# Kernel optimization log

Hardware: AMD Instinct MI355X
Metric: run time of the kernel (lower is better)

The kernel has to match this reference:

```python
import jax, jax.numpy as jnp
import numpy as np

N_NODES = 8192
N_EDGES = 262144
IN_DIM = 128
HID = 128
FLAT = N_NODES * HID  # 1048576


def gcn_conv(x, edge_index, W, b):
    """PyG-style GCNConv: add self-loops, symmetric deg^{-1/2} normalization,
    out[col] += norm * (x @ W)[row], plus bias."""
    N = x.shape[0]
    loop = jnp.arange(N)
    row = jnp.concatenate([edge_index[0], loop])  # source nodes
    col = jnp.concatenate([edge_index[1], loop])  # target nodes
    deg = jax.ops.segment_sum(jnp.ones_like(col, dtype=x.dtype), col, num_segments=N)
    dinv = jax.lax.rsqrt(jnp.maximum(deg, 1.0))  # deg >= 1 thanks to self-loops
    norm = dinv[row] * dinv[col]  # [E+N]
    h = x @ W  # [N, out]
    msg = h[row] * norm[:, None]  # gather
    out = jax.ops.segment_sum(msg, col, num_segments=N)  # scatter-add
    return out + b


def setup_inputs() -> dict:
    key = jax.random.key(0)
    ks = jax.random.split(key, 12)
    def lin(k, fan_in, shape):
        bound = 1.0 / np.sqrt(fan_in)
        return jax.random.uniform(k, shape, jnp.float32, -bound, bound)
    return {
        "x": jax.random.normal(ks[0], (N_NODES, IN_DIM), jnp.float32),
        "edge_index": jax.random.randint(ks[1], (2, N_EDGES), 0, N_NODES, jnp.int64 if jax.config.jax_enable_x64 else jnp.int32),
        "W1": lin(ks[2], IN_DIM, (IN_DIM, HID)),
        "b1": lin(ks[3], IN_DIM, (HID,)),
        "W2": lin(ks[4], HID, (HID, HID)),
        "b2": lin(ks[5], HID, (HID,)),
        "fc1_w": lin(ks[6], FLAT, (FLAT, HID)),
        "fc1_b": lin(ks[7], FLAT, (HID,)),
        "fc2_w": lin(ks[8], HID, (HID, HID)),
        "fc2_b": lin(ks[9], HID, (HID,)),
        "fc3_w": lin(ks[10], HID, (HID, 1)),
        "fc3_b": lin(ks[11], HID, (1,)),
    }


def reference(x, edge_index, W1, b1, W2, b2, fc1_w, fc1_b, fc2_w, fc2_b, fc3_w, fc3_b):
    e = jax.nn.relu(gcn_conv(x, edge_index, W1, b1))
    e = gcn_conv(e, edge_index, W2, b2)
    flat = e.reshape(-1)  # [N_NODES*HID]
    h = jax.nn.relu(flat @ fc1_w + fc1_b)
    h = jax.nn.relu(h @ fc2_w + fc2_b)
    q = h @ fc3_w + fc3_b  # [1]
    return q
```

## Files before the change

kernel.cpp:

```cpp
#include <hip/hip_runtime.h>

#define N_NODES 8192
#define N_EDGES 262144
#define DIM 128

__global__ void k_deg(const int* __restrict__ col, int* __restrict__ deg) {
    int e = blockIdx.x * blockDim.x + threadIdx.x;
    if (e < N_EDGES) atomicAdd(&deg[col[e]], 1);
}

__global__ __launch_bounds__(1024) void k_scan(const int* __restrict__ deg,
                                               int* __restrict__ rowptr,
                                               float* __restrict__ dinv) {
    __shared__ int part[1024];
    int t = threadIdx.x;
    int base = t * 8;
    int v[8];
    int s = 0;
    #pragma unroll
    for (int i = 0; i < 8; ++i) {
        int d = deg[base + i];
        dinv[base + i] = rsqrtf((float)d + 1.0f);
        v[i] = s; s += d;
    }
    part[t] = s;
    __syncthreads();
    for (int off = 1; off < 1024; off <<= 1) {
        int x = (t >= off) ? part[t - off] : 0;
        __syncthreads();
        part[t] += x;
        __syncthreads();
    }
    int basesum = (t == 0) ? 0 : part[t - 1];
    #pragma unroll
    for (int i = 0; i < 8; ++i) rowptr[base + i] = basesum + v[i];
    if (t == 1023) rowptr[8192] = part[1023];
}

__global__ void k_fill(const int* __restrict__ rows, const int* __restrict__ cols,
                       const int* __restrict__ rowptr, int* __restrict__ cnt,
                       int* __restrict__ srcs) {
    int e = blockIdx.x * blockDim.x + threadIdx.x;
    if (e < N_EDGES) {
        int c = cols[e];
        int p = atomicAdd(&cnt[c], 1);
        srcs[rowptr[c] + p] = rows[e];
    }
}

__global__ __launch_bounds__(256) void k_gemm(const float* __restrict__ x,
                                              const float* __restrict__ W,
                                              const float* __restrict__ dinv,
                                              float* __restrict__ out) {
    __shared__ float4 Wl[128 * 32];
    int t = threadIdx.x;
    const float4* W4 = (const float4*)W;
    for (int i = t; i < 128 * 32; i += 256) Wl[i] = W4[i];
    __syncthreads();

    int q  = t & 31;
    int rg = t >> 5;
    int row0 = blockIdx.x * 32;
    for (int p = 0; p < 4; ++p) {
        int row = row0 + p * 8 + rg;
        const float4* xr = (const float4*)(x + (size_t)row * DIM);
        float4 acc = {0.f, 0.f, 0.f, 0.f};
        #pragma unroll
        for (int k4 = 0; k4 < 32; ++k4) {
            float4 xv = xr[k4];
            float4 w0 = Wl[(k4 * 4 + 0) * 32 + q];
            float4 w1 = Wl[(k4 * 4 + 1) * 32 + q];
            float4 w2 = Wl[(k4 * 4 + 2) * 32 + q];
            float4 w3 = Wl[(k4 * 4 + 3) * 32 + q];
            acc.x += xv.x * w0.x + xv.y * w1.x + xv.z * w2.x + xv.w * w3.x;
            acc.y += xv.x * w0.y + xv.y * w1.y + xv.z * w2.y + xv.w * w3.y;
            acc.z += xv.x * w0.z + xv.y * w1.z + xv.z * w2.z + xv.w * w3.z;
            acc.w += xv.x * w0.w + xv.y * w1.w + xv.z * w2.w + xv.w * w3.w;
        }
        float s = dinv[row];
        acc.x *= s; acc.y *= s; acc.z *= s; acc.w *= s;
        ((float4*)(out + (size_t)row * DIM))[q] = acc;
    }
}

__global__ __launch_bounds__(256) void k_gather(const float* __restrict__ h,
                                                const int* __restrict__ srcs,
                                                const int* __restrict__ rowptr,
                                                const float* __restrict__ dinv,
                                                const float* __restrict__ b,
                                                float* __restrict__ out) {
    int t = threadIdx.x;
    int lane = t & 63;
    int node = blockIdx.x * 4 + (t >> 6);
    const float2* H = (const float2*)h;
    int beg = rowptr[node];
    int end = rowptr[node + 1];
    float2 acc = H[(size_t)node * 64 + lane];
    int j = beg;
    for (; j + 3 < end; j += 4) {
        int r0 = srcs[j], r1 = srcs[j + 1], r2 = srcs[j + 2], r3 = srcs[j + 3];
        float2 v0 = H[(size_t)r0 * 64 + lane];
        float2 v1 = H[(size_t)r1 * 64 + lane];
        float2 v2 = H[(size_t)r2 * 64 + lane];
        float2 v3 = H[(size_t)r3 * 64 + lane];
        acc.x += (v0.x + v1.x) + (v2.x + v3.x);
        acc.y += (v0.y + v1.y) + (v2.y + v3.y);
    }
    for (; j < end; ++j) {
        int r = srcs[j];
        float2 v = H[(size_t)r * 64 + lane];
        acc.x += v.x; acc.y += v.y;
    }
    float s = dinv[node];
    float2 bv = ((const float2*)b)[lane];
    float2 o;
    o.x = fmaxf(s * acc.x + bv.x, 0.f);
    o.y = fmaxf(s * acc.y + bv.y, 0.f);
    ((float2*)(out + (size_t)node * DIM))[lane] = o;
}

__global__ __launch_bounds__(256) void k_gfc(const float* __restrict__ h,
                                             const int* __restrict__ srcs,
                                             const int* __restrict__ rowptr,
                                             const float* __restrict__ dinv,
                                             const float* __restrict__ b,
                                             const float* __restrict__ w,
                                             float* __restrict__ facc) {
    __shared__ float oL[4][128];
    __shared__ float4 red4[4][32];
    int t = threadIdx.x;
    int lane = t & 63;
    int wid = t >> 6;
    int node = blockIdx.x * 4 + wid;
    const float2* H = (const float2*)h;
    int beg = rowptr[node];
    int end = rowptr[node + 1];
    float2 acc = H[(size_t)node * 64 + lane];
    int j = beg;
    for (; j + 3 < end; j += 4) {
        int r0 = srcs[j], r1 = srcs[j + 1], r2 = srcs[j + 2], r3 = srcs[j + 3];
        float2 v0 = H[(size_t)r0 * 64 + lane];
        float2 v1 = H[(size_t)r1 * 64 + lane];
        float2 v2 = H[(size_t)r2 * 64 + lane];
        float2 v3 = H[(size_t)r3 * 64 + lane];
        acc.x += (v0.x + v1.x) + (v2.x + v3.x);
        acc.y += (v0.y + v1.y) + (v2.y + v3.y);
    }
    for (; j < end; ++j) {
        int r = srcs[j];
        float2 v = H[(size_t)r * 64 + lane];
        acc.x += v.x; acc.y += v.y;
    }
    float s = dinv[node];
    float2 bv = ((const float2*)b)[lane];
    float2 o = { s * acc.x + bv.x, s * acc.y + bv.y };
    ((float2*)oL[wid])[lane] = o;
    __syncthreads();

    int q  = lane & 31;
    int kh = lane >> 5;
    size_t rowbase = (size_t)node * 128;
    float4 a4 = {0.f, 0.f, 0.f, 0.f};
    #pragma unroll 8
    for (int k2 = 0; k2 < 64; ++k2) {
        int k = k2 * 2 + kh;
        float ok = oL[wid][k];
        float4 wr = ((const float4*)(w + (rowbase + k) * 128))[q];
        a4.x += ok * wr.x;
        a4.y += ok * wr.y;
        a4.z += ok * wr.z;
        a4.w += ok * wr.w;
    }
    a4.x += __shfl_xor(a4.x, 32);
    a4.y += __shfl_xor(a4.y, 32);
    a4.z += __shfl_xor(a4.z, 32);
    a4.w += __shfl_xor(a4.w, 32);
    if (lane < 32) red4[wid][q] = a4;
    __syncthreads();
    if (t < 128) {
        const float* rf = (const float*)red4;
        float val = (rf[t] + rf[128 + t]) + (rf[256 + t] + rf[384 + t]);
        atomicAdd(&facc[t], val);
    }
}

__global__ __launch_bounds__(128) void k_tail(const float* __restrict__ facc,
                                              const float* __restrict__ fc1_b,
                                              const float* __restrict__ fc2_w,
                                              const float* __restrict__ fc2_b,
                                              const float* __restrict__ fc3_w,
                                              const float* __restrict__ fc3_b,
                                              float* __restrict__ out) {
    __shared__ float h1[128], red[128];
    int j = threadIdx.x;
    h1[j] = fmaxf(facc[j] + fc1_b[j], 0.f);
    __syncthreads();
    float a = 0.f;
    #pragma unroll 8
    for (int k = 0; k < 128; ++k) a += h1[k] * fc2_w[k * 128 + j];
    float h2 = fmaxf(a + fc2_b[j], 0.f);
    red[j] = h2 * fc3_w[j];
    __syncthreads();
    if (j == 0) {
        float s = 0.f;
        for (int k = 0; k < 128; ++k) s += red[k];
        out[0] = s + fc3_b[0];
    }
}

extern "C" void kernel_launch(void* const* d_in, const int* in_sizes, int n_in,
                              void* d_out, int out_size, void* d_ws, size_t ws_size,
                              hipStream_t stream) {
    const float* x     = (const float*)d_in[0];
    const int*   ei    = (const int*)d_in[1];
    const float* W1    = (const float*)d_in[2];
    const float* b1    = (const float*)d_in[3];
    const float* W2    = (const float*)d_in[4];
    const float* b2    = (const float*)d_in[5];
    const float* fc1_w = (const float*)d_in[6];
    const float* fc1_b = (const float*)d_in[7];
    const float* fc2_w = (const float*)d_in[8];
    const float* fc2_b = (const float*)d_in[9];
    const float* fc3_w = (const float*)d_in[10];
    const float* fc3_b = (const float*)d_in[11];
    const int* rows = ei;
    const int* cols = ei + N_EDGES;

    float* buf0   = (float*)d_ws;
    float* buf1   = buf0 + (size_t)N_NODES * DIM;
    int*   degi   = (int*)(buf1 + (size_t)N_NODES * DIM);
    int*   cnt    = degi + N_NODES;
    float* facc   = (float*)(cnt + N_NODES);
    float* dinv   = facc + DIM;
    int*   rowptr = (int*)(dinv + N_NODES);
    int*   srcs   = rowptr + N_NODES + 8;
    float* out    = (float*)d_out;

    hipMemsetAsync(degi, 0, (2 * N_NODES) * sizeof(int) + DIM * sizeof(float), stream);

    k_deg<<<N_EDGES / 256, 256, 0, stream>>>(cols, degi);
    k_scan<<<1, 1024, 0, stream>>>(degi, rowptr, dinv);
    k_fill<<<N_EDGES / 256, 256, 0, stream>>>(rows, cols, rowptr, cnt, srcs);

    k_gemm<<<N_NODES / 32, 256, 0, stream>>>(x, W1, dinv, buf0);
    k_gather<<<N_NODES / 4, 256, 0, stream>>>(buf0, srcs, rowptr, dinv, b1, buf1);

    k_gemm<<<N_NODES / 32, 256, 0, stream>>>(buf1, W2, dinv, buf0);
    k_gfc<<<N_NODES / 4, 256, 0, stream>>>(buf0, srcs, rowptr, dinv, b2, fc1_w, facc);

    k_tail<<<1, 128, 0, stream>>>(facc, fc1_b, fc2_w, fc2_b, fc3_w, fc3_b, out);
}
```

Baseline: 870.2 us.

## Replicate fc1 accumulators, stream weights nontemporally, vectorize gather, and use wave-level scan

Atomic adds from all 2048 blocks into one 128-float accumulator are spread over 64 replicas, which the tail kernel sums, to reduce atomic contention. The 512MB fc1 weight stream is read with nontemporal loads so it does not pollute the caches. The neighbor gather is factored into a helper that aligns the start, loads indices as int4 and keeps two accumulators. The single-block scan now uses wave shuffles in place of a shared-memory Hillis-Steele loop. Risks are extra memset and tail work, and different float summation order.

Result: faster. 838.9 us, median of 2 (-3.6%).

```diff
diff --git a/kernel.cpp b/kernel.cpp
--- a/kernel.cpp
+++ b/kernel.cpp
@@ -3,6 +3,9 @@
 #define N_NODES 8192
 #define N_EDGES 262144
 #define DIM 128
+#define NREP 64
+
+typedef float fv4 __attribute__((ext_vector_type(4)));
 
 __global__ void k_deg(const int* __restrict__ col, int* __restrict__ deg) {
     int e = blockIdx.x * blockDim.x + threadIdx.x;
@@ -12,7 +15,8 @@
 __global__ __launch_bounds__(1024) void k_scan(const int* __restrict__ deg,
                                                int* __restrict__ rowptr,
                                                float* __restrict__ dinv) {
-    __shared__ int part[1024];
+    __shared__ int wsum[16];
+    __shared__ int wpre[16];
     int t = threadIdx.x;
     int base = t * 8;
     int v[8];
@@ -23,18 +27,25 @@
         dinv[base + i] = rsqrtf((float)d + 1.0f);
         v[i] = s; s += d;
     }
-    part[t] = s;
-    __syncthreads();
-    for (int off = 1; off < 1024; off <<= 1) {
-        int x = (t >= off) ? part[t - off] : 0;
-        __syncthreads();
-        part[t] += x;
-        __syncthreads();
-    }
-    int basesum = (t == 0) ? 0 : part[t - 1];
-    #pragma unroll
-    for (int i = 0; i < 8; ++i) rowptr[base + i] = basesum + v[i];
-    if (t == 1023) rowptr[8192] = part[1023];
+    int lane = t & 63, wv = t >> 6;
+    int incl = s;
+    #pragma unroll
+    for (int off = 1; off < 64; off <<= 1) {
+        int n = __shfl_up(incl, off);
+        if (lane >= off) incl += n;
+    }
+    if (lane == 63) wsum[wv] = incl;
+    __syncthreads();
+    if (t == 0) {
+        int a = 0;
+        #pragma unroll
+        for (int i = 0; i < 16; ++i) { wpre[i] = a; a += wsum[i]; }
+        rowptr[8192] = a;
+    }
+    __syncthreads();
+    int ebase = wpre[wv] + incl - s;
+    #pragma unroll
+    for (int i = 0; i < 8; ++i) rowptr[base + i] = ebase + v[i];
 }
 
 __global__ void k_fill(const int* __restrict__ rows, const int* __restrict__ cols,
@@ -83,6 +94,35 @@
     }
 }
 
+__device__ __forceinline__ float2 gather_row(const float2* __restrict__ H,
+                                             const int* __restrict__ srcs,
+                                             int beg, int end, int node, int lane) {
+    float2 a0 = H[(size_t)node * 64 + lane];
+    float2 a1 = {0.f, 0.f};
+    int j = beg;
+    int npre = (4 - (beg & 3)) & 3;
+    if (npre > end - beg) npre = end - beg;
+    for (int p = 0; p < npre; ++p, ++j) {
+        float2 v = H[(size_t)srcs[j] * 64 + lane];
+        a0.x += v.x; a0.y += v.y;
+    }
+    for (; j + 3 < end; j += 4) {
+        int4 s4 = *reinterpret_cast<const int4*>(srcs + j);
+        float2 v0 = H[(size_t)s4.x * 64 + lane];
+        float2 v1 = H[(size_t)s4.y * 64 + lane];
+        float2 v2 = H[(size_t)s4.z * 64 + lane];
+        float2 v3 = H[(size_t)s4.w * 64 + lane];
+        a0.x += v0.x + v2.x; a0.y += v0.y + v2.y;
+        a1.x += v1.x + v3.x; a1.y += v1.y + v3.y;
+    }
+    for (; j < end; ++j) {
+        float2 v = H[(size_t)srcs[j] * 64 + lane];
+        a1.x += v.x; a1.y += v.y;
+    }
+    a0.x += a1.x; a0.y += a1.y;
+    return a0;
+}
+
 __global__ __launch_bounds__(256) void k_gather(const float* __restrict__ h,
                                                 const int* __restrict__ srcs,
                                                 const int* __restrict__ rowptr,
@@ -92,25 +132,7 @@
     int t = threadIdx.x;
     int lane = t & 63;
     int node = blockIdx.x * 4 + (t >> 6);
-    const float2* H = (const float2*)h;
-    int beg = rowptr[node];
-    int end = rowptr[node + 1];
-    float2 acc = H[(size_t)node * 64 + lane];
-    int j = beg;
-    for (; j + 3 < end; j += 4) {
-        int r0 = srcs[j], r1 = srcs[j + 1], r2 = srcs[j + 2], r3 = srcs[j + 3];
-        float2 v0 = H[(size_t)r0 * 64 + lane];
-        float2 v1 = H[(size_t)r1 * 64 + lane];
-        float2 v2 = H[(size_t)r2 * 64 + lane];
-        float2 v3 = H[(size_t)r3 * 64 + lane];
-        acc.x += (v0.x + v1.x) + (v2.x + v3.x);
-        acc.y += (v0.y + v1.y) + (v2.y + v3.y);
-    }
-    for (; j < end; ++j) {
-        int r = srcs[j];
-        float2 v = H[(size_t)r * 64 + lane];
-        acc.x += v.x; acc.y += v.y;
-    }
+    float2 acc = gather_row((const float2*)h, srcs, rowptr[node], rowptr[node + 1], node, lane);
     float s = dinv[node];
     float2 bv = ((const float2*)b)[lane];
     float2 o;
@@ -125,32 +147,14 @@
                                              const float* __restrict__ dinv,
                                              const float* __restrict__ b,
                                              const float* __restrict__ w,
-                                             float* __restrict__ facc) {
+                                             float* __restrict__ facc_r) {
     __shared__ float oL[4][128];
-    __shared__ float4 red4[4][32];
+    __shared__ fv4 red4[4][32];
     int t = threadIdx.x;
     int lane = t & 63;
     int wid = t >> 6;
     int node = blockIdx.x * 4 + wid;
-    const float2* H = (const float2*)h;
-    int beg = rowptr[node];
-    int end = rowptr[node + 1];
-    float2 acc = H[(size_t)node * 64 + lane];
-    int j = beg;
-    for (; j + 3 < end; j += 4) {
-        int r0 = srcs[j], r1 = srcs[j + 1], r2 = srcs[j + 2], r3 = srcs[j + 3];
-        float2 v0 = H[(size_t)r0 * 64 + lane];
-        float2 v1 = H[(size_t)r1 * 64 + lane];
-        float2 v2 = H[(size_t)r2 * 64 + lane];
-        float2 v3 = H[(size_t)r3 * 64 + lane];
-        acc.x += (v0.x + v1.x) + (v2.x + v3.x);
-        acc.y += (v0.y + v1.y) + (v2.y + v3.y);
-    }
-    for (; j < end; ++j) {
-        int r = srcs[j];
-        float2 v = H[(size_t)r * 64 + lane];
-        acc.x += v.x; acc.y += v.y;
-    }
+    float2 acc = gather_row((const float2*)h, srcs, rowptr[node], rowptr[node + 1], node, lane);
     float s = dinv[node];
     float2 bv = ((const float2*)b)[lane];
     float2 o = { s * acc.x + bv.x, s * acc.y + bv.y };
@@ -160,16 +164,14 @@
     int q  = lane & 31;
     int kh = lane >> 5;
     size_t rowbase = (size_t)node * 128;
-    float4 a4 = {0.f, 0.f, 0.f, 0.f};
+    fv4 a4 = {0.f, 0.f, 0.f, 0.f};
     #pragma unroll 8
     for (int k2 = 0; k2 < 64; ++k2) {
         int k = k2 * 2 + kh;
         float ok = oL[wid][k];
-        float4 wr = ((const float4*)(w + (rowbase + k) * 128))[q];
-        a4.x += ok * wr.x;
-        a4.y += ok * wr.y;
-        a4.z += ok * wr.z;
-        a4.w += ok * wr.w;
+        const fv4* wp = (const fv4*)(w + (rowbase + k) * 128);
+        fv4 wr = __builtin_nontemporal_load(wp + q);
+        a4 += ok * wr;
     }
     a4.x += __shfl_xor(a4.x, 32);
     a4.y += __shfl_xor(a4.y, 32);
@@ -180,11 +182,11 @@
     if (t < 128) {
         const float* rf = (const float*)red4;
         float val = (rf[t] + rf[128 + t]) + (rf[256 + t] + rf[384 + t]);
-        atomicAdd(&facc[t], val);
-    }
-}
-
-__global__ __launch_bounds__(128) void k_tail(const float* __restrict__ facc,
+        atomicAdd(&facc_r[((blockIdx.x & (NREP - 1)) << 7) + t], val);
+    }
+}
+
+__global__ __launch_bounds__(128) void k_tail(const float* __restrict__ facc_r,
                                               const float* __restrict__ fc1_b,
                                               const float* __restrict__ fc2_w,
                                               const float* __restrict__ fc2_b,
@@ -193,7 +195,10 @@
                                               float* __restrict__ out) {
     __shared__ float h1[128], red[128];
     int j = threadIdx.x;
-    h1[j] = fmaxf(facc[j] + fc1_b[j], 0.f);
+    float a0 = 0.f;
+    #pragma unroll
+    for (int r = 0; r < NREP; ++r) a0 += facc_r[r * 128 + j];
+    h1[j] = fmaxf(a0 + fc1_b[j], 0.f);
     __syncthreads();
     float a = 0.f;
     #pragma unroll 8
@@ -230,13 +235,13 @@
     float* buf1   = buf0 + (size_t)N_NODES * DIM;
     int*   degi   = (int*)(buf1 + (size_t)N_NODES * DIM);
     int*   cnt    = degi + N_NODES;
-    float* facc   = (float*)(cnt + N_NODES);
-    float* dinv   = facc + DIM;
+    float* facc_r = (float*)(cnt + N_NODES);
+    float* dinv   = facc_r + NREP * DIM;
     int*   rowptr = (int*)(dinv + N_NODES);
     int*   srcs   = rowptr + N_NODES + 8;
     float* out    = (float*)d_out;
 
-    hipMemsetAsync(degi, 0, (2 * N_NODES) * sizeof(int) + DIM * sizeof(float), stream);
+    hipMemsetAsync(degi, 0, (2 * N_NODES) * sizeof(int) + NREP * DIM * sizeof(float), stream);
 
     k_deg<<<N_EDGES / 256, 256, 0, stream>>>(cols, degi);
     k_scan<<<1, 1024, 0, stream>>>(degi, rowptr, dinv);
@@ -246,7 +251,7 @@
     k_gather<<<N_NODES / 4, 256, 0, stream>>>(buf0, srcs, rowptr, dinv, b1, buf1);
 
     k_gemm<<<N_NODES / 32, 256, 0, stream>>>(buf1, W2, dinv, buf0);
-    k_gfc<<<N_NODES / 4, 256, 0, stream>>>(buf0, srcs, rowptr, dinv, b2, fc1_w, facc);
-
-    k_tail<<<1, 128, 0, stream>>>(facc, fc1_b, fc2_w, fc2_b, fc3_w, fc3_b, out);
-}
+    k_gfc<<<N_NODES / 4, 256, 0, stream>>>(buf0, srcs, rowptr, dinv, b2, fc1_w, facc_r);
+
+    k_tail<<<1, 128, 0, stream>>>(facc_r, fc1_b, fc2_w, fc2_b, fc3_w, fc3_b, out);
+}
```
